# Kernel tuning notes

Measured on AMD Instinct MI355X. Metric: run time of the kernel, lower is better.

## Reference

```python
import jax, jax.numpy as jnp
import numpy as np

# hyper_params (mode='test')
PRE_NMS = 1000
POST_NMS = 300
IOU_TH = 0.7
VARIANCES = np.array([0.1, 0.1, 0.2, 0.2], dtype=np.float32)
FM = 64            # feature map height/width
ANCHOR_COUNT = 9   # 3 scales x 3 ratios


def _make_anchors():
    """Normalized [y1,x1,y2,x2] anchors on a FM x FM grid, 9 per cell."""
    scales = np.array([0.1, 0.2, 0.4], np.float32)
    ratios = np.array([0.5, 1.0, 2.0], np.float32)
    ws = (scales[:, None] * np.sqrt(ratios)[None, :]).reshape(-1)  # (9,)
    hs = (scales[:, None] / np.sqrt(ratios)[None, :]).reshape(-1)  # (9,)
    ctr = (np.arange(FM, dtype=np.float32) + 0.5) / FM
    cy, cx = np.meshgrid(ctr, ctr, indexing='ij')                  # (FM,FM)
    cy = cy[..., None]; cx = cx[..., None]                         # (FM,FM,1)
    anchors = np.stack([cy - 0.5 * hs, cx - 0.5 * ws,
                        cy + 0.5 * hs, cx + 0.5 * ws], axis=-1)    # (FM,FM,9,4)
    return jnp.asarray(anchors.reshape(-1, 4))                     # (36864,4)


def setup_inputs() -> dict:
    key = jax.random.key(0)
    k1, k2 = jax.random.split(key)
    B = 16
    rpn_bbox_deltas = jax.random.normal(k1, (B, FM, FM, ANCHOR_COUNT * 4), dtype=jnp.float32)
    rpn_labels = jax.random.uniform(k2, (B, FM, FM, ANCHOR_COUNT), dtype=jnp.float32)
    return {"rpn_bbox_deltas": rpn_bbox_deltas,
            "rpn_labels": rpn_labels,
            "anchors": _make_anchors()}


def _nms_single(boxes):
    """Greedy NMS on score-sorted boxes (N,4) -> (POST_NMS,4), zero-padded."""
    N = boxes.shape[0]
    y1, x1, y2, x2 = boxes[:, 0], boxes[:, 1], boxes[:, 2], boxes[:, 3]
    area = (y2 - y1) * (x2 - x1)                                   # (N,)
    iy1 = jnp.maximum(y1[:, None], y1[None, :])
    ix1 = jnp.maximum(x1[:, None], x1[None, :])
    iy2 = jnp.minimum(y2[:, None], y2[None, :])
    ix2 = jnp.minimum(x2[:, None], x2[None, :])
    inter = jnp.maximum(iy2 - iy1, 0.0) * jnp.maximum(ix2 - ix1, 0.0)
    iou = inter / jnp.maximum(area[:, None] + area[None, :] - inter, 1e-9)  # (N,N)
    idx = jnp.arange(N)

    def body(i, keep):
        # if box i survives, suppress later boxes with high overlap
        suppress = keep[i] & (iou[i] > IOU_TH) & (idx > i)
        return keep & ~suppress

    keep = jax.lax.fori_loop(0, N, body, jnp.ones((N,), dtype=bool))
    # stable sort: kept boxes first, original (score-descending) order preserved
    order = jnp.argsort(jnp.where(keep, 0, 1))[:POST_NMS]
    sel = boxes[order]
    valid = keep[order]
    # combined_non_max_suppression clips output boxes to [0,1] and zero-pads
    return jnp.where(valid[:, None], jnp.clip(sel, 0.0, 1.0), 0.0)


def reference(rpn_bbox_deltas, rpn_labels, anchors):
    B = rpn_bbox_deltas.shape[0]
    N = anchors.shape[0]
    deltas = rpn_bbox_deltas.reshape(B, N, 4) * jnp.asarray(VARIANCES)
    labels = rpn_labels.reshape(B, N)

    # decode deltas against anchors
    anc_h = anchors[:, 2] - anchors[:, 0]
    anc_w = anchors[:, 3] - anchors[:, 1]
    anc_cy = anchors[:, 0] + 0.5 * anc_h
    anc_cx = anchors[:, 1] + 0.5 * anc_w
    h = jnp.exp(deltas[..., 2]) * anc_h
    w = jnp.exp(deltas[..., 3]) * anc_w
    cy = deltas[..., 0] * anc_h + anc_cy
    cx = deltas[..., 1] * anc_w + anc_cx
    boxes = jnp.stack([cy - 0.5 * h, cx - 0.5 * w,
                       cy + 0.5 * h, cx + 0.5 * w], axis=-1)       # (B,N,4)

    # top-k by objectness score (descending, so NMS input is pre-sorted)
    _, pre_idx = jax.lax.top_k(labels, PRE_NMS)                    # (B,PRE_NMS)
    pre_boxes = jnp.take_along_axis(boxes, pre_idx[..., None], axis=1)  # (B,PRE_NMS,4)

    roi_bboxes = jax.vmap(_nms_single)(pre_boxes)                  # (B,POST_NMS,4)
    return jax.lax.stop_gradient(roi_bboxes)
```

## Files before the change

### kernel.cpp

```cpp
#include <hip/hip_runtime.h>
#include <stdint.h>

#pragma clang fp contract(off)

#define FM 64
#define AC 9
#define N_ANCH (FM * FM * AC)
#define PRE_NMS 1000
#define POST_NMS 300
#define SEL_CAP 1024
#define NWAVE 16

#define SLICES 16
#define K1_NT 256
#define SLICE_KEYS (N_ANCH / SLICES)
#define KEYS_PT (SLICE_KEYS / K1_NT)
#define SLICE_TOP 128
#define COMPACT_CAP 192
#define MERGE_CAP (SLICES * SLICE_TOP)

#define NCOPY 8
#define HSTR 257

#define M_WSTRIDE 1024
#define M_WORDS_PER_B (16 * M_WSTRIDE)
#define WS_BOX_FLOATS_PER_B (5 * SEL_CAP)

__device__ __forceinline__ uint32_t mono_key(float v) {
    uint32_t u = __float_as_uint(v);
    return (u & 0x80000000u) ? ~u : (u | 0x80000000u);
}

__device__ __forceinline__ float clip01(float x) {
    return fminf(fmaxf(x, 0.0f), 1.0f);
}

__device__ __forceinline__ uint64_t bcast64(uint64_t v, int srclane) {
    uint32_t lo = (uint32_t)v, hi = (uint32_t)(v >> 32);
    lo = __builtin_amdgcn_readlane(lo, srclane);
    hi = __builtin_amdgcn_readlane(hi, srclane);
    return ((uint64_t)hi << 32) | (uint64_t)lo;
}

__device__ __forceinline__ void scan256(const uint32_t* __restrict__ h, uint32_t K,
                                        uint32_t* shm, uint32_t& outBin, uint32_t& outKrem) {
    const int t    = threadIdx.x;
    const int lane = t & 63;
    const int wv   = t >> 6;
    const uint32_t q = h[t];
    uint32_t sfx = q, o;
    o = __shfl_down(sfx, 1);  if (lane < 63) sfx += o;
    o = __shfl_down(sfx, 2);  if (lane < 62) sfx += o;
    o = __shfl_down(sfx, 4);  if (lane < 60) sfx += o;
    o = __shfl_down(sfx, 8);  if (lane < 56) sfx += o;
    o = __shfl_down(sfx, 16); if (lane < 48) sfx += o;
    o = __shfl_down(sfx, 32); if (lane < 32) sfx += o;
    if (lane == 0) shm[wv] = sfx;
    __syncthreads();
    uint32_t wAbove = 0;
    for (int w2 = wv + 1; w2 < 4; ++w2) wAbove += shm[w2];
    const uint32_t above = wAbove + (sfx - q);
    if ((above < K) && (above + q >= K)) { shm[4] = (uint32_t)t; shm[5] = K - above; }
    __syncthreads();
    outBin  = shm[4];
    outKrem = shm[5];
}

__global__ __launch_bounds__(K1_NT) void k1s_slice_top(
    const float* __restrict__ labels,
    uint64_t* __restrict__ wsCand)
{
    const int s = blockIdx.x;
    const int b = blockIdx.y;
    const int t = threadIdx.x;
    const int lane = t & 63;

    __shared__ uint32_t hc[NCOPY * HSTR];
    __shared__ uint32_t red[256];
    __shared__ uint32_t shm[8];
    __shared__ uint64_t cand[COMPACT_CAP];
    __shared__ uint32_t scnt;

    const float* lab = labels + (size_t)b * N_ANCH + (size_t)s * SLICE_KEYS;
    uint32_t key[KEYS_PT];
#pragma unroll
    for (int r = 0; r < KEYS_PT; ++r)
        key[r] = mono_key(lab[r * K1_NT + t]);

    for (int i = t; i < NCOPY * HSTR; i += K1_NT) hc[i] = 0u;
    if (t == 0) scnt = 0u;
    __syncthreads();

    const int cbase = (lane & 7) * HSTR;
#pragma unroll
    for (int r = 0; r < KEYS_PT; ++r)
        atomicAdd(&hc[cbase + (key[r] >> 24)], 1u);
    __syncthreads();
    uint32_t sum = 0;
#pragma unroll
    for (int c = 0; c < NCOPY; ++c) sum += hc[c * HSTR + t];
    red[t] = sum;
    __syncthreads();
    uint32_t b0, krem;
    scan256(red, SLICE_TOP, shm, b0, krem);
    __syncthreads();

    red[t] = 0u;
    __syncthreads();
#pragma unroll
    for (int r = 0; r < KEYS_PT; ++r)
        if ((key[r] >> 24) == b0) atomicAdd(&red[(key[r] >> 16) & 0xFFu], 1u);
    __syncthreads();
    uint32_t b1, krem2;
    scan256(red, krem, shm, b1, krem2);
    const uint32_t thresh16 = (b0 << 8) | b1;

#pragma unroll
    for (int r = 0; r < KEYS_PT; ++r) {
        const uint32_t u = key[r];
        if ((u >> 16) >= thresh16) {
            const uint32_t gi = (uint32_t)(s * SLICE_KEYS + r * K1_NT + t);
            uint32_t pos = atomicAdd(&scnt, 1u);
            if (pos < COMPACT_CAP)
                cand[pos] = ((uint64_t)u << 32) | (uint64_t)(0xFFFFFFFFu - gi);
        }
    }
    __syncthreads();
    uint32_t c = scnt; if (c > COMPACT_CAP) c = COMPACT_CAP;
    if (t >= (int)c && t < COMPACT_CAP) cand[t] = 0ull;
    __syncthreads();

    if (t < COMPACT_CAP) {
        const uint64_t mine = cand[t];
        uint32_t rank = 0;
        for (int i = 0; i < COMPACT_CAP; i += 4) {
            rank += (cand[i]     > mine) + (cand[i + 1] > mine)
                  + (cand[i + 2] > mine) + (cand[i + 3] > mine);
        }
        if (t < (int)c && rank < SLICE_TOP)
            wsCand[((size_t)b * SLICES + s) * SLICE_TOP + rank] = mine;
    }
}

__global__ __launch_bounds__(K1_NT) void k1m_merge_decode(
    const float* __restrict__ deltas,
    const float* __restrict__ anchors,
    const uint64_t* __restrict__ wsCand,
    float* __restrict__ wsBox)
{
    const int chunk = blockIdx.x;
    const int b     = blockIdx.y;
    const int t     = threadIdx.x;

    __shared__ uint64_t keyA[MERGE_CAP];
    const uint64_t* c2 = wsCand + (size_t)b * MERGE_CAP;
    for (int i = t; i < MERGE_CAP; i += K1_NT) keyA[i] = c2[i];
    __syncthreads();

    if (t < SLICE_TOP) {
        const uint64_t mine = keyA[chunk * SLICE_TOP + t];
        uint32_t rank = 0;
#pragma unroll
        for (int r = 0; r < SLICES; ++r) {
            const uint64_t* a = &keyA[r * SLICE_TOP];
            uint32_t lo = 0;
#pragma unroll
            for (uint32_t s2 = 128; s2 > 0; s2 >>= 1)
                if (lo + s2 <= 128u && a[lo + s2 - 1] > mine) lo += s2;
            rank += lo;
        }
        if (rank < PRE_NMS) {
            uint32_t idx = 0xFFFFFFFFu - (uint32_t)(mine & 0xFFFFFFFFull);
            float4 d4 = *(const float4*)(deltas + ((size_t)b * N_ANCH + idx) * 4);
            float4 a4 = *(const float4*)(anchors + (size_t)idx * 4);
            float anc_h  = a4.z - a4.x;
            float anc_w  = a4.w - a4.y;
            float anc_cy = a4.x + 0.5f * anc_h;
            float anc_cx = a4.y + 0.5f * anc_w;
            float dy = d4.x * 0.1f, dx = d4.y * 0.1f;
            float dh = d4.z * 0.2f, dw = d4.w * 0.2f;
            float h  = expf(dh) * anc_h;
            float w  = expf(dw) * anc_w;
            float cy = dy * anc_h + anc_cy;
            float cx = dx * anc_w + anc_cx;
            float y1 = cy - 0.5f * h, x1 = cx - 0.5f * w;
            float y2 = cy + 0.5f * h, x2 = cx + 0.5f * w;
            float* wb = wsBox + (size_t)b * WS_BOX_FLOATS_PER_B;
            wb[rank]              = y1;
            wb[SEL_CAP + rank]    = x1;
            wb[2*SEL_CAP + rank]  = y2;
            wb[3*SEL_CAP + rank]  = x2;
            wb[4*SEL_CAP + rank]  = (y2 - y1) * (x2 - x1);
        }
    }
}

__global__ __launch_bounds__(1024) void k2_iou_matrix(
    const float* __restrict__ wsBox,
    uint64_t* __restrict__ wsM)
{
    const int gx   = blockIdx.x;
    const int b    = blockIdx.y;
    const int t    = threadIdx.x;
    const int lane = t & 63;
    const int wave = t >> 6;

    int cb, r0, r1;
    if (gx < 16) { cb = gx;     r0 = 0;   r1 = 64 * (cb + 1); if (r1 > 512) r1 = 512; }
    else         { cb = gx - 8; r0 = 512; r1 = 64 * (cb + 1); }
    if (r1 > PRE_NMS) r1 = PRE_NMS;

    __shared__ float s[5 * SEL_CAP];
    const float4* b4 = (const float4*)(wsBox + (size_t)b * WS_BOX_FLOATS_PER_B);
    float4* s4 = (float4*)s;
    for (int i = t; i < (5 * SEL_CAP) / 4; i += 1024) s4[i] = b4[i];
    __syncthreads();

    float* ly1 = s;
    float* lx1 = s + SEL_CAP;
    float* ly2 = s + 2 * SEL_CAP;
    float* lx2 = s + 3 * SEL_CAP;
    float* lar = s + 4 * SEL_CAP;

    const int j = cb * 64 + lane;
    const float y1j = ly1[j], x1j = lx1[j], y2j = ly2[j], x2j = lx2[j], aj = lar[j];

    uint64_t* Mb = wsM + (size_t)b * M_WORDS_PER_B + (size_t)cb * M_WSTRIDE;
    for (int i = r0 + wave; i < r1; i += NWAVE) {
        float iy1 = fmaxf(ly1[i], y1j);
        float ix1 = fmaxf(lx1[i], x1j);
        float iy2 = fminf(ly2[i], y2j);
        float ix2 = fminf(lx2[i], x2j);
        float ih = iy2 - iy1; if (ih < 0.f) ih = 0.f;
        float iw = ix2 - ix1; if (iw < 0.f) iw = 0.f;
        float inter = ih * iw;
        float denom = lar[i] + aj - inter;
        if (denom < 1e-9f) denom = 1e-9f;
        float iou = inter / denom;
        bool sup = (j > i) && (iou > 0.7f);
        uint64_t mask = __ballot(sup ? 1 : 0);
        if (lane == 0) Mb[i] = mask;
    }
}

__global__ __launch_bounds__(1024) void k3_reduce_out(
    const float* __restrict__ wsBox,
    const uint64_t* __restrict__ wsM,
    float* __restrict__ out)
{
    const int b    = blockIdx.x;
    const int t    = threadIdx.x;
    const int lane = t & 63;
    const int wave = t >> 6;

    __shared__ uint64_t remv[16];
    __shared__ uint64_t keepW[16];
    __shared__ uint32_t wordPref[16];

    const uint64_t* Mg = wsM + (size_t)b * M_WORDS_PER_B;

    if (t < 16) remv[t] = 0ull;
    __syncthreads();

    for (int w = 0; w < 16; ++w) {
        if (wave == 0) {
            const uint64_t m = Mg[(size_t)w * M_WSTRIDE + 64 * w + lane];
            uint64_t cur = remv[w];
            if (w < 15) {
#pragma unroll
                for (int bp = 0; bp < 64; ++bp) {
                    const uint64_t mb = bcast64(m, bp);
                    cur |= ((cur >> bp) & 1ull) ? 0ull : mb;
                }
            } else {
#pragma unroll
                for (int bp = 0; bp < 40; ++bp) {
                    const uint64_t mb = bcast64(m, bp);
                    cur |= ((cur >> bp) & 1ull) ? 0ull : mb;
                }
            }
            const uint64_t valid = (w == 15) ? ((1ull << 40) - 1ull) : ~0ull;
            if (lane == 0) keepW[w] = (~cur) & valid;
        }
        __syncthreads();
        if (wave > w) {
            const uint64_t km = keepW[w];
            uint64_t v = Mg[(size_t)wave * M_WSTRIDE + 64 * w + lane];
            v = ((km >> lane) & 1ull) ? v : 0ull;
            v |= __shfl_xor(v, 32);
            v |= __shfl_xor(v, 16);
            v |= __shfl_xor(v, 8);
            v |= __shfl_xor(v, 4);
            v |= __shfl_xor(v, 2);
            v |= __shfl_xor(v, 1);
            if (lane == 0) remv[wave] |= v;
        }
        __syncthreads();
    }

    if (t == 0) {
        uint32_t acc = 0u;
        for (int w = 0; w < 16; ++w) {
            wordPref[w] = acc;
            acc += (uint32_t)__popcll(keepW[w]);
        }
    }
    float* ob = out + (size_t)b * (POST_NMS * 4);
    for (int i = t; i < POST_NMS * 4; i += 1024) ob[i] = 0.0f;
    __syncthreads();

    if (t < PRE_NMS) {
        const int w = t >> 6, bpos = t & 63;
        uint64_t kw = keepW[w];
        if ((kw >> bpos) & 1ull) {
            uint32_t rank = wordPref[w] +
                            (uint32_t)__popcll(kw & ((1ull << bpos) - 1ull));
            if (rank < POST_NMS) {
                const float* wb = wsBox + (size_t)b * WS_BOX_FLOATS_PER_B;
                float* o = ob + (size_t)rank * 4;
                o[0] = clip01(wb[t]);
                o[1] = clip01(wb[SEL_CAP + t]);
                o[2] = clip01(wb[2*SEL_CAP + t]);
                o[3] = clip01(wb[3*SEL_CAP + t]);
            }
        }
    }
}

extern "C" void kernel_launch(void* const* d_in, const int* in_sizes, int n_in,
                              void* d_out, int out_size, void* d_ws, size_t ws_size,
                              hipStream_t stream) {
    const float* deltas  = (const float*)d_in[0];
    const float* labels  = (const float*)d_in[1];
    const float* anchors = (const float*)d_in[2];
    float* out = (float*)d_out;
    const int B = in_sizes[1] / N_ANCH;

    char* p = (char*)d_ws;
    uint64_t* wsCand = (uint64_t*)p;
    float*    wsBox  = (float*)(p + (size_t)B * MERGE_CAP * 8);
    uint64_t* wsM    = (uint64_t*)(p + (size_t)B * MERGE_CAP * 8
                                     + (size_t)B * WS_BOX_FLOATS_PER_B * 4);

    k1s_slice_top<<<dim3(SLICES, B), K1_NT, 0, stream>>>(labels, wsCand);
    k1m_merge_decode<<<dim3(SLICES, B), K1_NT, 0, stream>>>(deltas, anchors, wsCand, wsBox);
    k2_iou_matrix<<<dim3(24, B), 1024, 0, stream>>>(wsBox, wsM);
    k3_reduce_out<<<B, 1024, 0, stream>>>(wsBox, wsM, out);
}
```

Baseline: 131.0 us.

## Fuse top-k, decode, IoU and NMS reduce into one flag-synchronised kernel

Merges the four separate launches into one kernel with 16 blocks per image. The stages are ordered by per-image global flags that each block writes with release stores and polls with acquire loads. The aim is to remove launch gaps and let different images progress independently. The IoU stage also shrinks from 1024-thread blocks to 256-thread blocks, which lowers per-image parallelism. The flags are set to a magic value and never cleared, so repeated calls on the same workspace could pass the waits early unless the workspace is zeroed between calls.

```diff
diff --git a/kernel.cpp b/kernel.cpp
--- a/kernel.cpp
+++ b/kernel.cpp
@@ -3,28 +3,28 @@
 
 #pragma clang fp contract(off)
 
-#define FM 64
-#define AC 9
-#define N_ANCH (FM * FM * AC)
+#define N_ANCH 36864
 #define PRE_NMS 1000
 #define POST_NMS 300
 #define SEL_CAP 1024
-#define NWAVE 16
+#define NT 256
 
 #define SLICES 16
-#define K1_NT 256
-#define SLICE_KEYS (N_ANCH / SLICES)
-#define KEYS_PT (SLICE_KEYS / K1_NT)
+#define SLICE_KEYS 2304
+#define KEYS_PT 9
 #define SLICE_TOP 128
 #define COMPACT_CAP 192
-#define MERGE_CAP (SLICES * SLICE_TOP)
+#define MERGE_CAP 2048
 
 #define NCOPY 8
 #define HSTR 257
 
 #define M_WSTRIDE 1024
-#define M_WORDS_PER_B (16 * M_WSTRIDE)
-#define WS_BOX_FLOATS_PER_B (5 * SEL_CAP)
+#define M_WORDS_PER_B 16384
+#define WS_BOX_FLOATS_PER_B 5120
+
+#define MAGIC 0x5CA1AB1Eu
+#define SMEM_BYTES 20992
 
 __device__ __forceinline__ uint32_t mono_key(float v) {
     uint32_t u = __float_as_uint(v);
@@ -40,6 +40,27 @@
     lo = __builtin_amdgcn_readlane(lo, srclane);
     hi = __builtin_amdgcn_readlane(hi, srclane);
     return ((uint64_t)hi << 32) | (uint64_t)lo;
+}
+
+__device__ __forceinline__ void signal(uint32_t* f) {
+    __syncthreads();
+    if (threadIdx.x == 0) {
+        __threadfence();
+        __hip_atomic_store(f, MAGIC, __ATOMIC_RELEASE, __HIP_MEMORY_SCOPE_AGENT);
+    }
+}
+
+__device__ __forceinline__ void wait16(const uint32_t* fbase) {
+    const int t = threadIdx.x;
+    int ok;
+    do {
+        ok = 1;
+        if (t < 16)
+            ok = (__hip_atomic_load(&fbase[t], __ATOMIC_ACQUIRE,
+                                    __HIP_MEMORY_SCOPE_AGENT) == MAGIC);
+        else
+            __builtin_amdgcn_s_sleep(2);
+    } while (!__syncthreads_and(ok));
 }
 
 __device__ __forceinline__ void scan256(const uint32_t* __restrict__ h, uint32_t K,
@@ -66,262 +87,256 @@
     outKrem = shm[5];
 }
 
-__global__ __launch_bounds__(K1_NT) void k1s_slice_top(
+__global__ __launch_bounds__(NT) void fused_roibbox(
+    const float* __restrict__ deltas,
     const float* __restrict__ labels,
-    uint64_t* __restrict__ wsCand)
+    const float* __restrict__ anchors,
+    float* __restrict__ out,
+    uint64_t* __restrict__ wsCand,
+    float* __restrict__ wsBox,
+    uint64_t* __restrict__ wsM,
+    uint32_t* __restrict__ wsFlag,
+    int nB)
 {
-    const int s = blockIdx.x;
-    const int b = blockIdx.y;
-    const int t = threadIdx.x;
-    const int lane = t & 63;
-
-    __shared__ uint32_t hc[NCOPY * HSTR];
-    __shared__ uint32_t red[256];
-    __shared__ uint32_t shm[8];
-    __shared__ uint64_t cand[COMPACT_CAP];
-    __shared__ uint32_t scnt;
-
-    const float* lab = labels + (size_t)b * N_ANCH + (size_t)s * SLICE_KEYS;
-    uint32_t key[KEYS_PT];
-#pragma unroll
-    for (int r = 0; r < KEYS_PT; ++r)
-        key[r] = mono_key(lab[r * K1_NT + t]);
-
-    for (int i = t; i < NCOPY * HSTR; i += K1_NT) hc[i] = 0u;
-    if (t == 0) scnt = 0u;
-    __syncthreads();
-
-    const int cbase = (lane & 7) * HSTR;
-#pragma unroll
-    for (int r = 0; r < KEYS_PT; ++r)
-        atomicAdd(&hc[cbase + (key[r] >> 24)], 1u);
-    __syncthreads();
-    uint32_t sum = 0;
-#pragma unroll
-    for (int c = 0; c < NCOPY; ++c) sum += hc[c * HSTR + t];
-    red[t] = sum;
-    __syncthreads();
-    uint32_t b0, krem;
-    scan256(red, SLICE_TOP, shm, b0, krem);
-    __syncthreads();
-
-    red[t] = 0u;
-    __syncthreads();
-#pragma unroll
-    for (int r = 0; r < KEYS_PT; ++r)
-        if ((key[r] >> 24) == b0) atomicAdd(&red[(key[r] >> 16) & 0xFFu], 1u);
-    __syncthreads();
-    uint32_t b1, krem2;
-    scan256(red, krem, shm, b1, krem2);
-    const uint32_t thresh16 = (b0 << 8) | b1;
-
-#pragma unroll
-    for (int r = 0; r < KEYS_PT; ++r) {
-        const uint32_t u = key[r];
-        if ((u >> 16) >= thresh16) {
-            const uint32_t gi = (uint32_t)(s * SLICE_KEYS + r * K1_NT + t);
-            uint32_t pos = atomicAdd(&scnt, 1u);
-            if (pos < COMPACT_CAP)
-                cand[pos] = ((uint64_t)u << 32) | (uint64_t)(0xFFFFFFFFu - gi);
-        }
-    }
-    __syncthreads();
-    uint32_t c = scnt; if (c > COMPACT_CAP) c = COMPACT_CAP;
-    if (t >= (int)c && t < COMPACT_CAP) cand[t] = 0ull;
-    __syncthreads();
-
-    if (t < COMPACT_CAP) {
-        const uint64_t mine = cand[t];
-        uint32_t rank = 0;
-        for (int i = 0; i < COMPACT_CAP; i += 4) {
-            rank += (cand[i]     > mine) + (cand[i + 1] > mine)
-                  + (cand[i + 2] > mine) + (cand[i + 3] > mine);
-        }
-        if (t < (int)c && rank < SLICE_TOP)
-            wsCand[((size_t)b * SLICES + s) * SLICE_TOP + rank] = mine;
-    }
-}
-
-__global__ __launch_bounds__(K1_NT) void k1m_merge_decode(
-    const float* __restrict__ deltas,
-    const float* __restrict__ anchors,
-    const uint64_t* __restrict__ wsCand,
-    float* __restrict__ wsBox)
-{
-    const int chunk = blockIdx.x;
-    const int b     = blockIdx.y;
+    extern __shared__ char sm[];
+    const int bid   = blockIdx.x;
+    const int chunk = bid & 15;
+    const int b     = bid >> 4;
     const int t     = threadIdx.x;
-
-    __shared__ uint64_t keyA[MERGE_CAP];
-    const uint64_t* c2 = wsCand + (size_t)b * MERGE_CAP;
-    for (int i = t; i < MERGE_CAP; i += K1_NT) keyA[i] = c2[i];
-    __syncthreads();
-
-    if (t < SLICE_TOP) {
-        const uint64_t mine = keyA[chunk * SLICE_TOP + t];
-        uint32_t rank = 0;
-#pragma unroll
-        for (int r = 0; r < SLICES; ++r) {
-            const uint64_t* a = &keyA[r * SLICE_TOP];
-            uint32_t lo = 0;
-#pragma unroll
-            for (uint32_t s2 = 128; s2 > 0; s2 >>= 1)
-                if (lo + s2 <= 128u && a[lo + s2 - 1] > mine) lo += s2;
-            rank += lo;
-        }
-        if (rank < PRE_NMS) {
-            uint32_t idx = 0xFFFFFFFFu - (uint32_t)(mine & 0xFFFFFFFFull);
-            float4 d4 = *(const float4*)(deltas + ((size_t)b * N_ANCH + idx) * 4);
-            float4 a4 = *(const float4*)(anchors + (size_t)idx * 4);
-            float anc_h  = a4.z - a4.x;
-            float anc_w  = a4.w - a4.y;
-            float anc_cy = a4.x + 0.5f * anc_h;
-            float anc_cx = a4.y + 0.5f * anc_w;
-            float dy = d4.x * 0.1f, dx = d4.y * 0.1f;
-            float dh = d4.z * 0.2f, dw = d4.w * 0.2f;
-            float h  = expf(dh) * anc_h;
-            float w  = expf(dw) * anc_w;
-            float cy = dy * anc_h + anc_cy;
-            float cx = dx * anc_w + anc_cx;
-            float y1 = cy - 0.5f * h, x1 = cx - 0.5f * w;
-            float y2 = cy + 0.5f * h, x2 = cx + 0.5f * w;
-            float* wb = wsBox + (size_t)b * WS_BOX_FLOATS_PER_B;
-            wb[rank]              = y1;
-            wb[SEL_CAP + rank]    = x1;
-            wb[2*SEL_CAP + rank]  = y2;
-            wb[3*SEL_CAP + rank]  = x2;
-            wb[4*SEL_CAP + rank]  = (y2 - y1) * (x2 - x1);
-        }
-    }
-}
-
-__global__ __launch_bounds__(1024) void k2_iou_matrix(
-    const float* __restrict__ wsBox,
-    uint64_t* __restrict__ wsM)
-{
-    const int gx   = blockIdx.x;
-    const int b    = blockIdx.y;
-    const int t    = threadIdx.x;
-    const int lane = t & 63;
-    const int wave = t >> 6;
-
-    int cb, r0, r1;
-    if (gx < 16) { cb = gx;     r0 = 0;   r1 = 64 * (cb + 1); if (r1 > 512) r1 = 512; }
-    else         { cb = gx - 8; r0 = 512; r1 = 64 * (cb + 1); }
-    if (r1 > PRE_NMS) r1 = PRE_NMS;
-
-    __shared__ float s[5 * SEL_CAP];
-    const float4* b4 = (const float4*)(wsBox + (size_t)b * WS_BOX_FLOATS_PER_B);
-    float4* s4 = (float4*)s;
-    for (int i = t; i < (5 * SEL_CAP) / 4; i += 1024) s4[i] = b4[i];
-    __syncthreads();
-
-    float* ly1 = s;
-    float* lx1 = s + SEL_CAP;
-    float* ly2 = s + 2 * SEL_CAP;
-    float* lx2 = s + 3 * SEL_CAP;
-    float* lar = s + 4 * SEL_CAP;
-
-    const int j = cb * 64 + lane;
-    const float y1j = ly1[j], x1j = lx1[j], y2j = ly2[j], x2j = lx2[j], aj = lar[j];
-
-    uint64_t* Mb = wsM + (size_t)b * M_WORDS_PER_B + (size_t)cb * M_WSTRIDE;
-    for (int i = r0 + wave; i < r1; i += NWAVE) {
-        float iy1 = fmaxf(ly1[i], y1j);
-        float ix1 = fmaxf(lx1[i], x1j);
-        float iy2 = fminf(ly2[i], y2j);
-        float ix2 = fminf(lx2[i], x2j);
-        float ih = iy2 - iy1; if (ih < 0.f) ih = 0.f;
-        float iw = ix2 - ix1; if (iw < 0.f) iw = 0.f;
-        float inter = ih * iw;
-        float denom = lar[i] + aj - inter;
-        if (denom < 1e-9f) denom = 1e-9f;
-        float iou = inter / denom;
-        bool sup = (j > i) && (iou > 0.7f);
-        uint64_t mask = __ballot(sup ? 1 : 0);
-        if (lane == 0) Mb[i] = mask;
-    }
-}
-
-__global__ __launch_bounds__(1024) void k3_reduce_out(
-    const float* __restrict__ wsBox,
-    const uint64_t* __restrict__ wsM,
-    float* __restrict__ out)
-{
-    const int b    = blockIdx.x;
-    const int t    = threadIdx.x;
-    const int lane = t & 63;
-    const int wave = t >> 6;
-
-    __shared__ uint64_t remv[16];
-    __shared__ uint64_t keepW[16];
-    __shared__ uint32_t wordPref[16];
-
-    const uint64_t* Mg = wsM + (size_t)b * M_WORDS_PER_B;
-
-    if (t < 16) remv[t] = 0ull;
-    __syncthreads();
-
-    for (int w = 0; w < 16; ++w) {
-        if (wave == 0) {
-            const uint64_t m = Mg[(size_t)w * M_WSTRIDE + 64 * w + lane];
-            uint64_t cur = remv[w];
-            if (w < 15) {
-#pragma unroll
-                for (int bp = 0; bp < 64; ++bp) {
-                    const uint64_t mb = bcast64(m, bp);
-                    cur |= ((cur >> bp) & 1ull) ? 0ull : mb;
+    const int lane  = t & 63;
+    const int wave  = t >> 6;
+
+    uint32_t* flagA = wsFlag + b * 16;
+    uint32_t* flagB = wsFlag + (nB + b) * 16;
+    uint32_t* flagC = wsFlag + (2 * nB + b) * 16;
+
+    {
+        uint32_t* hc   = (uint32_t*)sm;
+        uint32_t* red  = (uint32_t*)(sm + 8224);
+        uint32_t* shm  = (uint32_t*)(sm + 9248);
+        uint64_t* cand = (uint64_t*)(sm + 9280);
+        uint32_t* scnt = (uint32_t*)(sm + 10816);
+
+        const float* lab = labels + (size_t)b * N_ANCH + (size_t)chunk * SLICE_KEYS;
+        uint32_t key[KEYS_PT];
+#pragma unroll
+        for (int r = 0; r < KEYS_PT; ++r)
+            key[r] = mono_key(lab[r * NT + t]);
+
+        for (int i = t; i < NCOPY * HSTR; i += NT) hc[i] = 0u;
+        if (t == 0) *scnt = 0u;
+        __syncthreads();
+
+        const int cbase = (lane & 7) * HSTR;
+#pragma unroll
+        for (int r = 0; r < KEYS_PT; ++r)
+            atomicAdd(&hc[cbase + (key[r] >> 24)], 1u);
+        __syncthreads();
+        uint32_t sum = 0;
+#pragma unroll
+        for (int c = 0; c < NCOPY; ++c) sum += hc[c * HSTR + t];
+        red[t] = sum;
+        __syncthreads();
+        uint32_t b0, krem;
+        scan256(red, SLICE_TOP, shm, b0, krem);
+        __syncthreads();
+
+        red[t] = 0u;
+        __syncthreads();
+#pragma unroll
+        for (int r = 0; r < KEYS_PT; ++r)
+            if ((key[r] >> 24) == b0) atomicAdd(&red[(key[r] >> 16) & 0xFFu], 1u);
+        __syncthreads();
+        uint32_t b1, krem2;
+        scan256(red, krem, shm, b1, krem2);
+        const uint32_t thresh16 = (b0 << 8) | b1;
+
+#pragma unroll
+        for (int r = 0; r < KEYS_PT; ++r) {
+            const uint32_t u = key[r];
+            if ((u >> 16) >= thresh16) {
+                const uint32_t gi = (uint32_t)(chunk * SLICE_KEYS + r * NT + t);
+                uint32_t pos = atomicAdd(scnt, 1u);
+                if (pos < COMPACT_CAP)
+                    cand[pos] = ((uint64_t)u << 32) | (uint64_t)(0xFFFFFFFFu - gi);
+            }
+        }
+        __syncthreads();
+        uint32_t c = *scnt; if (c > COMPACT_CAP) c = COMPACT_CAP;
+        if (t >= (int)c && t < COMPACT_CAP) cand[t] = 0ull;
+        __syncthreads();
+
+        if (t < COMPACT_CAP) {
+            const uint64_t mine = cand[t];
+            uint32_t rank = 0;
+            for (int i = 0; i < COMPACT_CAP; i += 4)
+                rank += (cand[i]     > mine) + (cand[i + 1] > mine)
+                      + (cand[i + 2] > mine) + (cand[i + 3] > mine);
+            if (t < (int)c && rank < SLICE_TOP)
+                wsCand[((size_t)b * SLICES + chunk) * SLICE_TOP + rank] = mine;
+        }
+    }
+    signal(&flagA[chunk]);
+
+    wait16(flagA);
+    {
+        uint64_t* keyA = (uint64_t*)sm;
+        const uint64_t* c2 = wsCand + (size_t)b * MERGE_CAP;
+        for (int i = t; i < MERGE_CAP; i += NT) keyA[i] = c2[i];
+        __syncthreads();
+
+        if (t < SLICE_TOP) {
+            const uint64_t mine = keyA[chunk * SLICE_TOP + t];
+            uint32_t rank = 0;
+#pragma unroll
+            for (int r = 0; r < SLICES; ++r) {
+                const uint64_t* a = &keyA[r * SLICE_TOP];
+                uint32_t lo = 0;
+#pragma unroll
+                for (uint32_t s2 = 128; s2 > 0; s2 >>= 1)
+                    if (lo + s2 <= 128u && a[lo + s2 - 1] > mine) lo += s2;
+                rank += lo;
+            }
+            if (rank < PRE_NMS) {
+                uint32_t idx = 0xFFFFFFFFu - (uint32_t)(mine & 0xFFFFFFFFull);
+                float4 d4 = *(const float4*)(deltas + ((size_t)b * N_ANCH + idx) * 4);
+                float4 a4 = *(const float4*)(anchors + (size_t)idx * 4);
+                float anc_h  = a4.z - a4.x;
+                float anc_w  = a4.w - a4.y;
+                float anc_cy = a4.x + 0.5f * anc_h;
+                float anc_cx = a4.y + 0.5f * anc_w;
+                float dy = d4.x * 0.1f, dx = d4.y * 0.1f;
+                float dh = d4.z * 0.2f, dw = d4.w * 0.2f;
+                float h  = expf(dh) * anc_h;
+                float w  = expf(dw) * anc_w;
+                float cy = dy * anc_h + anc_cy;
+                float cx = dx * anc_w + anc_cx;
+                float y1 = cy - 0.5f * h, x1 = cx - 0.5f * w;
+                float y2 = cy + 0.5f * h, x2 = cx + 0.5f * w;
+                float* wb = wsBox + (size_t)b * WS_BOX_FLOATS_PER_B;
+                wb[rank]              = y1;
+                wb[SEL_CAP + rank]    = x1;
+                wb[2*SEL_CAP + rank]  = y2;
+                wb[3*SEL_CAP + rank]  = x2;
+                wb[4*SEL_CAP + rank]  = (y2 - y1) * (x2 - x1);
+            }
+        }
+    }
+    signal(&flagB[chunk]);
+
+    wait16(flagB);
+    {
+        float* sbox = (float*)sm;
+        const float4* b4 = (const float4*)(wsBox + (size_t)b * WS_BOX_FLOATS_PER_B);
+        float4* s4 = (float4*)sbox;
+        for (int i = t; i < WS_BOX_FLOATS_PER_B / 4; i += NT) s4[i] = b4[i];
+        __syncthreads();
+
+        float* ly1 = sbox;
+        float* lx1 = sbox + SEL_CAP;
+        float* ly2 = sbox + 2 * SEL_CAP;
+        float* lx2 = sbox + 3 * SEL_CAP;
+        float* lar = sbox + 4 * SEL_CAP;
+
+        const int j = chunk * 64 + lane;
+        const float y1j = ly1[j], x1j = lx1[j], y2j = ly2[j], x2j = lx2[j], aj = lar[j];
+
+        int r1 = 64 * (chunk + 1);
+        if (r1 > PRE_NMS) r1 = PRE_NMS;
+        uint64_t* Mb = wsM + (size_t)b * M_WORDS_PER_B + (size_t)chunk * M_WSTRIDE;
+
+        for (int i = wave; i < r1; i += 4) {
+            float iy1 = fmaxf(ly1[i], y1j);
+            float ix1 = fmaxf(lx1[i], x1j);
+            float iy2 = fminf(ly2[i], y2j);
+            float ix2 = fminf(lx2[i], x2j);
+            float ih = iy2 - iy1; if (ih < 0.f) ih = 0.f;
+            float iw = ix2 - ix1; if (iw < 0.f) iw = 0.f;
+            float inter = ih * iw;
+            float denom = lar[i] + aj - inter;
+            if (denom < 1e-9f) denom = 1e-9f;
+            float iou = inter / denom;
+            bool sup = (j > i) && (iou > 0.7f);
+            uint64_t mask = __ballot(sup ? 1 : 0);
+            if (lane == 0) Mb[i] = mask;
+        }
+    }
+    signal(&flagC[chunk]);
+
+    if (chunk != 0) return;
+    wait16(flagC);
+    {
+        uint64_t* remv     = (uint64_t*)sm;
+        uint64_t* keepW    = remv + 16;
+        uint32_t* wordPref = (uint32_t*)(keepW + 16);
+
+        const uint64_t* Mg = wsM + (size_t)b * M_WORDS_PER_B;
+        if (t < 16) remv[t] = 0ull;
+        __syncthreads();
+
+        for (int w = 0; w < 16; ++w) {
+            if (wave == 0) {
+                const uint64_t m = Mg[(size_t)w * M_WSTRIDE + 64 * w + lane];
+                uint64_t cur = remv[w];
+                if (w < 15) {
+#pragma unroll
+                    for (int bp = 0; bp < 64; ++bp) {
+                        const uint64_t mb = bcast64(m, bp);
+                        cur |= ((cur >> bp) & 1ull) ? 0ull : mb;
+                    }
+                } else {
+#pragma unroll
+                    for (int bp = 0; bp < 40; ++bp) {
+                        const uint64_t mb = bcast64(m, bp);
+                        cur |= ((cur >> bp) & 1ull) ? 0ull : mb;
+                    }
                 }
-            } else {
-#pragma unroll
-                for (int bp = 0; bp < 40; ++bp) {
-                    const uint64_t mb = bcast64(m, bp);
-                    cur |= ((cur >> bp) & 1ull) ? 0ull : mb;
+                const uint64_t valid = (w == 15) ? ((1ull << 40) - 1ull) : ~0ull;
+                if (lane == 0) keepW[w] = (~cur) & valid;
+            }
+            __syncthreads();
+            if (wave > 0) {
+                const uint64_t km = keepW[w];
+                for (int w2 = w + wave; w2 < 16; w2 += 3) {
+                    uint64_t v = Mg[(size_t)w2 * M_WSTRIDE + 64 * w + lane];
+                    v = ((km >> lane) & 1ull) ? v : 0ull;
+                    v |= __shfl_xor(v, 32);
+                    v |= __shfl_xor(v, 16);
+                    v |= __shfl_xor(v, 8);
+                    v |= __shfl_xor(v, 4);
+                    v |= __shfl_xor(v, 2);
+                    v |= __shfl_xor(v, 1);
+                    if (lane == 0) remv[w2] |= v;
                 }
             }
-            const uint64_t valid = (w == 15) ? ((1ull << 40) - 1ull) : ~0ull;
-            if (lane == 0) keepW[w] = (~cur) & valid;
-        }
-        __syncthreads();
-        if (wave > w) {
-            const uint64_t km = keepW[w];
-            uint64_t v = Mg[(size_t)wave * M_WSTRIDE + 64 * w + lane];
-            v = ((km >> lane) & 1ull) ? v : 0ull;
-            v |= __shfl_xor(v, 32);
-            v |= __shfl_xor(v, 16);
-            v |= __shfl_xor(v, 8);
-            v |= __shfl_xor(v, 4);
-            v |= __shfl_xor(v, 2);
-            v |= __shfl_xor(v, 1);
-            if (lane == 0) remv[wave] |= v;
-        }
-        __syncthreads();
-    }
-
-    if (t == 0) {
-        uint32_t acc = 0u;
-        for (int w = 0; w < 16; ++w) {
-            wordPref[w] = acc;
-            acc += (uint32_t)__popcll(keepW[w]);
-        }
-    }
-    float* ob = out + (size_t)b * (POST_NMS * 4);
-    for (int i = t; i < POST_NMS * 4; i += 1024) ob[i] = 0.0f;
-    __syncthreads();
-
-    if (t < PRE_NMS) {
-        const int w = t >> 6, bpos = t & 63;
-        uint64_t kw = keepW[w];
-        if ((kw >> bpos) & 1ull) {
-            uint32_t rank = wordPref[w] +
-                            (uint32_t)__popcll(kw & ((1ull << bpos) - 1ull));
-            if (rank < POST_NMS) {
-                const float* wb = wsBox + (size_t)b * WS_BOX_FLOATS_PER_B;
-                float* o = ob + (size_t)rank * 4;
-                o[0] = clip01(wb[t]);
-                o[1] = clip01(wb[SEL_CAP + t]);
-                o[2] = clip01(wb[2*SEL_CAP + t]);
-                o[3] = clip01(wb[3*SEL_CAP + t]);
+            __syncthreads();
+        }
+
+        if (t == 0) {
+            uint32_t acc = 0u;
+            for (int w = 0; w < 16; ++w) {
+                wordPref[w] = acc;
+                acc += (uint32_t)__popcll(keepW[w]);
+            }
+        }
+        float* ob = out + (size_t)b * (POST_NMS * 4);
+        for (int i = t; i < POST_NMS * 4; i += NT) ob[i] = 0.0f;
+        __syncthreads();
+
+        const float* wb = wsBox + (size_t)b * WS_BOX_FLOATS_PER_B;
+        for (int q = t; q < PRE_NMS; q += NT) {
+            const int w = q >> 6, bpos = q & 63;
+            uint64_t kw = keepW[w];
+            if ((kw >> bpos) & 1ull) {
+                uint32_t rank = wordPref[w] +
+                                (uint32_t)__popcll(kw & ((1ull << bpos) - 1ull));
+                if (rank < POST_NMS) {
+                    float* o = ob + (size_t)rank * 4;
+                    o[0] = clip01(wb[q]);
+                    o[1] = clip01(wb[SEL_CAP + q]);
+                    o[2] = clip01(wb[2*SEL_CAP + q]);
+                    o[3] = clip01(wb[3*SEL_CAP + q]);
+                }
             }
         }
     }
@@ -341,9 +356,10 @@
     float*    wsBox  = (float*)(p + (size_t)B * MERGE_CAP * 8);
     uint64_t* wsM    = (uint64_t*)(p + (size_t)B * MERGE_CAP * 8
                                      + (size_t)B * WS_BOX_FLOATS_PER_B * 4);
-
-    k1s_slice_top<<<dim3(SLICES, B), K1_NT, 0, stream>>>(labels, wsCand);
-    k1m_merge_decode<<<dim3(SLICES, B), K1_NT, 0, stream>>>(deltas, anchors, wsCand, wsBox);
-    k2_iou_matrix<<<dim3(24, B), 1024, 0, stream>>>(wsBox, wsM);
-    k3_reduce_out<<<B, 1024, 0, stream>>>(wsBox, wsM, out);
-}
+    uint32_t* wsFlag = (uint32_t*)(p + (size_t)B * MERGE_CAP * 8
+                                     + (size_t)B * WS_BOX_FLOATS_PER_B * 4
+                                     + (size_t)B * M_WORDS_PER_B * 8);
+
+    fused_roibbox<<<dim3(SLICES * B), dim3(NT), SMEM_BYTES, stream>>>(
+        deltas, labels, anchors, out, wsCand, wsBox, wsM, wsFlag, B);
+}
```

Result: slower. 205.5 us (+56.8%).

## Fuse merge-decode, IoU matrix and NMS reduction into one per-batch kernel

Applied to the files above, without the earlier changes.

Replaces three kernels (merge/decode, IoU bitmask, greedy reduce) with a single 1024-thread block per image that keeps candidate keys, decoded boxes and the full suppression bitmask in ~150KB of LDS. This removes two kernel launches and the global-memory round trips for boxes and the mask matrix. The cost is parallelism: only B=16 blocks run instead of 16×B and 24×B, so the IoU work is spread over far fewer CUs. It also adds a large LDS zero-fill.

```diff
diff --git a/kernel.cpp b/kernel.cpp
--- a/kernel.cpp
+++ b/kernel.cpp
@@ -3,9 +3,7 @@
 
 #pragma clang fp contract(off)
 
-#define FM 64
-#define AC 9
-#define N_ANCH (FM * FM * AC)
+#define N_ANCH 36864
 #define PRE_NMS 1000
 #define POST_NMS 300
 #define SEL_CAP 1024
@@ -13,18 +11,19 @@
 
 #define SLICES 16
 #define K1_NT 256
-#define SLICE_KEYS (N_ANCH / SLICES)
-#define KEYS_PT (SLICE_KEYS / K1_NT)
+#define SLICE_KEYS 2304
+#define KEYS_PT 9
 #define SLICE_TOP 128
 #define COMPACT_CAP 192
-#define MERGE_CAP (SLICES * SLICE_TOP)
+#define MERGE_CAP 2048
 
 #define NCOPY 8
 #define HSTR 257
 
-#define M_WSTRIDE 1024
-#define M_WORDS_PER_B (16 * M_WSTRIDE)
-#define WS_BOX_FLOATS_PER_B (5 * SEL_CAP)
+#define M_OFF   0
+#define BOX_OFF 131072
+#define SC_OFF  151552
+#define KBIG_SMEM 152064
 
 __device__ __forceinline__ uint32_t mono_key(float v) {
     uint32_t u = __float_as_uint(v);
@@ -133,32 +132,48 @@
     if (t < COMPACT_CAP) {
         const uint64_t mine = cand[t];
         uint32_t rank = 0;
-        for (int i = 0; i < COMPACT_CAP; i += 4) {
+        for (int i = 0; i < COMPACT_CAP; i += 4)
             rank += (cand[i]     > mine) + (cand[i + 1] > mine)
                   + (cand[i + 2] > mine) + (cand[i + 3] > mine);
-        }
         if (t < (int)c && rank < SLICE_TOP)
             wsCand[((size_t)b * SLICES + s) * SLICE_TOP + rank] = mine;
     }
 }
 
-__global__ __launch_bounds__(K1_NT) void k1m_merge_decode(
+__global__ __launch_bounds__(1024) void kbig(
     const float* __restrict__ deltas,
     const float* __restrict__ anchors,
     const uint64_t* __restrict__ wsCand,
-    float* __restrict__ wsBox)
+    float* __restrict__ out)
 {
-    const int chunk = blockIdx.x;
-    const int b     = blockIdx.y;
-    const int t     = threadIdx.x;
-
-    __shared__ uint64_t keyA[MERGE_CAP];
+    extern __shared__ char sm[];
+    uint64_t* Mlds  = (uint64_t*)sm;
+    float*    boxes = (float*)(sm + BOX_OFF);
+    uint64_t* remv  = (uint64_t*)(sm + SC_OFF);
+    uint64_t* keepW = remv + 16;
+    uint32_t* wordPref = (uint32_t*)(keepW + 16);
+    uint64_t* keyA  = Mlds;
+
+    const int b    = blockIdx.x;
+    const int t    = threadIdx.x;
+    const int lane = t & 63;
+    const int wave = t >> 6;
+
+    float* ly1 = boxes;
+    float* lx1 = boxes + SEL_CAP;
+    float* ly2 = boxes + 2 * SEL_CAP;
+    float* lx2 = boxes + 3 * SEL_CAP;
+    float* lar = boxes + 4 * SEL_CAP;
+
     const uint64_t* c2 = wsCand + (size_t)b * MERGE_CAP;
-    for (int i = t; i < MERGE_CAP; i += K1_NT) keyA[i] = c2[i];
-    __syncthreads();
-
-    if (t < SLICE_TOP) {
-        const uint64_t mine = keyA[chunk * SLICE_TOP + t];
+    keyA[t]        = c2[t];
+    keyA[t + 1024] = c2[t + 1024];
+    for (int i = t; i < 5 * SEL_CAP; i += 1024) boxes[i] = 0.f;
+    __syncthreads();
+
+#pragma unroll
+    for (int kk = 0; kk < 2; ++kk) {
+        const uint64_t mine = keyA[t + kk * 1024];
         uint32_t rank = 0;
 #pragma unroll
         for (int r = 0; r < SLICES; ++r) {
@@ -185,86 +200,50 @@
             float cx = dx * anc_w + anc_cx;
             float y1 = cy - 0.5f * h, x1 = cx - 0.5f * w;
             float y2 = cy + 0.5f * h, x2 = cx + 0.5f * w;
-            float* wb = wsBox + (size_t)b * WS_BOX_FLOATS_PER_B;
-            wb[rank]              = y1;
-            wb[SEL_CAP + rank]    = x1;
-            wb[2*SEL_CAP + rank]  = y2;
-            wb[3*SEL_CAP + rank]  = x2;
-            wb[4*SEL_CAP + rank]  = (y2 - y1) * (x2 - x1);
-        }
-    }
-}
-
-__global__ __launch_bounds__(1024) void k2_iou_matrix(
-    const float* __restrict__ wsBox,
-    uint64_t* __restrict__ wsM)
-{
-    const int gx   = blockIdx.x;
-    const int b    = blockIdx.y;
-    const int t    = threadIdx.x;
-    const int lane = t & 63;
-    const int wave = t >> 6;
-
-    int cb, r0, r1;
-    if (gx < 16) { cb = gx;     r0 = 0;   r1 = 64 * (cb + 1); if (r1 > 512) r1 = 512; }
-    else         { cb = gx - 8; r0 = 512; r1 = 64 * (cb + 1); }
-    if (r1 > PRE_NMS) r1 = PRE_NMS;
-
-    __shared__ float s[5 * SEL_CAP];
-    const float4* b4 = (const float4*)(wsBox + (size_t)b * WS_BOX_FLOATS_PER_B);
-    float4* s4 = (float4*)s;
-    for (int i = t; i < (5 * SEL_CAP) / 4; i += 1024) s4[i] = b4[i];
-    __syncthreads();
-
-    float* ly1 = s;
-    float* lx1 = s + SEL_CAP;
-    float* ly2 = s + 2 * SEL_CAP;
-    float* lx2 = s + 3 * SEL_CAP;
-    float* lar = s + 4 * SEL_CAP;
-
-    const int j = cb * 64 + lane;
-    const float y1j = ly1[j], x1j = lx1[j], y2j = ly2[j], x2j = lx2[j], aj = lar[j];
-
-    uint64_t* Mb = wsM + (size_t)b * M_WORDS_PER_B + (size_t)cb * M_WSTRIDE;
-    for (int i = r0 + wave; i < r1; i += NWAVE) {
-        float iy1 = fmaxf(ly1[i], y1j);
-        float ix1 = fmaxf(lx1[i], x1j);
-        float iy2 = fminf(ly2[i], y2j);
-        float ix2 = fminf(lx2[i], x2j);
-        float ih = iy2 - iy1; if (ih < 0.f) ih = 0.f;
-        float iw = ix2 - ix1; if (iw < 0.f) iw = 0.f;
-        float inter = ih * iw;
-        float denom = lar[i] + aj - inter;
-        if (denom < 1e-9f) denom = 1e-9f;
-        float iou = inter / denom;
-        bool sup = (j > i) && (iou > 0.7f);
-        uint64_t mask = __ballot(sup ? 1 : 0);
-        if (lane == 0) Mb[i] = mask;
-    }
-}
-
-__global__ __launch_bounds__(1024) void k3_reduce_out(
-    const float* __restrict__ wsBox,
-    const uint64_t* __restrict__ wsM,
-    float* __restrict__ out)
-{
-    const int b    = blockIdx.x;
-    const int t    = threadIdx.x;
-    const int lane = t & 63;
-    const int wave = t >> 6;
-
-    __shared__ uint64_t remv[16];
-    __shared__ uint64_t keepW[16];
-    __shared__ uint32_t wordPref[16];
-
-    const uint64_t* Mg = wsM + (size_t)b * M_WORDS_PER_B;
+            ly1[rank] = y1; lx1[rank] = x1; ly2[rank] = y2; lx2[rank] = x2;
+            lar[rank] = (y2 - y1) * (x2 - x1);
+        }
+    }
+    __syncthreads();
+
+    for (int i = t; i < 16 * 1024; i += 1024) Mlds[i] = 0ull;
+    __syncthreads();
+
+    {
+        const int p = wave >> 1, half = wave & 1;
+#pragma unroll
+        for (int sel = 0; sel < 2; ++sel) {
+            const int w = sel ? (15 - p) : p;
+            const int j = (w << 6) | lane;
+            const float y1j = ly1[j], x1j = lx1[j], y2j = ly2[j], x2j = lx2[j], aj = lar[j];
+            int rmax = (w + 1) << 6; if (rmax > PRE_NMS) rmax = PRE_NMS;
+            const int rbeg = half ? (rmax >> 1) : 0;
+            const int rend = half ? rmax : (rmax >> 1);
+            for (int i = rbeg; i < rend; ++i) {
+                float iy1 = fmaxf(ly1[i], y1j);
+                float ix1 = fmaxf(lx1[i], x1j);
+                float iy2 = fminf(ly2[i], y2j);
+                float ix2 = fminf(lx2[i], x2j);
+                float ih = iy2 - iy1; if (ih < 0.f) ih = 0.f;
+                float iw = ix2 - ix1; if (iw < 0.f) iw = 0.f;
+                float inter = ih * iw;
+                float denom = lar[i] + aj - inter;
+                if (denom < 1e-9f) denom = 1e-9f;
+                float iou = inter / denom;
+                bool sup = (j > i) && (iou > 0.7f);
+                uint64_t mask = __ballot(sup ? 1 : 0);
+                if (lane == 0) Mlds[(w << 10) + i] = mask;
+            }
+        }
+    }
+    __syncthreads();
 
     if (t < 16) remv[t] = 0ull;
     __syncthreads();
 
     for (int w = 0; w < 16; ++w) {
         if (wave == 0) {
-            const uint64_t m = Mg[(size_t)w * M_WSTRIDE + 64 * w + lane];
+            const uint64_t m = Mlds[(w << 10) + 64 * w + lane];
             uint64_t cur = remv[w];
             if (w < 15) {
 #pragma unroll
@@ -285,7 +264,7 @@
         __syncthreads();
         if (wave > w) {
             const uint64_t km = keepW[w];
-            uint64_t v = Mg[(size_t)wave * M_WSTRIDE + 64 * w + lane];
+            uint64_t v = Mlds[(wave << 10) + 64 * w + lane];
             v = ((km >> lane) & 1ull) ? v : 0ull;
             v |= __shfl_xor(v, 32);
             v |= __shfl_xor(v, 16);
@@ -316,12 +295,11 @@
             uint32_t rank = wordPref[w] +
                             (uint32_t)__popcll(kw & ((1ull << bpos) - 1ull));
             if (rank < POST_NMS) {
-                const float* wb = wsBox + (size_t)b * WS_BOX_FLOATS_PER_B;
                 float* o = ob + (size_t)rank * 4;
-                o[0] = clip01(wb[t]);
-                o[1] = clip01(wb[SEL_CAP + t]);
-                o[2] = clip01(wb[2*SEL_CAP + t]);
-                o[3] = clip01(wb[3*SEL_CAP + t]);
+                o[0] = clip01(ly1[t]);
+                o[1] = clip01(lx1[t]);
+                o[2] = clip01(ly2[t]);
+                o[3] = clip01(lx2[t]);
             }
         }
     }
@@ -336,14 +314,8 @@
     float* out = (float*)d_out;
     const int B = in_sizes[1] / N_ANCH;
 
-    char* p = (char*)d_ws;
-    uint64_t* wsCand = (uint64_t*)p;
-    float*    wsBox  = (float*)(p + (size_t)B * MERGE_CAP * 8);
-    uint64_t* wsM    = (uint64_t*)(p + (size_t)B * MERGE_CAP * 8
-                                     + (size_t)B * WS_BOX_FLOATS_PER_B * 4);
+    uint64_t* wsCand = (uint64_t*)d_ws;
 
     k1s_slice_top<<<dim3(SLICES, B), K1_NT, 0, stream>>>(labels, wsCand);
-    k1m_merge_decode<<<dim3(SLICES, B), K1_NT, 0, stream>>>(deltas, anchors, wsCand, wsBox);
-    k2_iou_matrix<<<dim3(24, B), 1024, 0, stream>>>(wsBox, wsM);
-    k3_reduce_out<<<B, 1024, 0, stream>>>(wsBox, wsM, out);
-}
+    kbig<<<B, 1024, KBIG_SMEM, stream>>>(deltas, anchors, wsCand, out);
+}
```

Result: slower. 273.9 us (+109.0%).

## Fuse merge-rank/decode into IOU matrix kernel, decoding boxes into shared memory

Applied to the files above, without the earlier changes.

Removes the separate merge/decode kernel. Each of the 24 IOU-matrix blocks per batch now recomputes the global rank of all 2048 candidates and decodes the top-1000 boxes straight into shared memory. Block 0 writes the box coordinates to the workspace for the final kernel. This drops one kernel launch and a global round trip of the box data, at the cost of redundant rank and decode work in every block. The area array is no longer written to the workspace, so k3 must not depend on it.

```diff
diff --git a/kernel.cpp b/kernel.cpp
--- a/kernel.cpp
+++ b/kernel.cpp
@@ -3,9 +3,7 @@
 
 #pragma clang fp contract(off)
 
-#define FM 64
-#define AC 9
-#define N_ANCH (FM * FM * AC)
+#define N_ANCH 36864
 #define PRE_NMS 1000
 #define POST_NMS 300
 #define SEL_CAP 1024
@@ -13,18 +11,18 @@
 
 #define SLICES 16
 #define K1_NT 256
-#define SLICE_KEYS (N_ANCH / SLICES)
-#define KEYS_PT (SLICE_KEYS / K1_NT)
+#define SLICE_KEYS 2304
+#define KEYS_PT 9
 #define SLICE_TOP 128
 #define COMPACT_CAP 192
-#define MERGE_CAP (SLICES * SLICE_TOP)
+#define MERGE_CAP 2048
 
 #define NCOPY 8
 #define HSTR 257
 
 #define M_WSTRIDE 1024
-#define M_WORDS_PER_B (16 * M_WSTRIDE)
-#define WS_BOX_FLOATS_PER_B (5 * SEL_CAP)
+#define M_WORDS_PER_B 16384
+#define WS_BOX_FLOATS_PER_B 5120
 
 __device__ __forceinline__ uint32_t mono_key(float v) {
     uint32_t u = __float_as_uint(v);
@@ -133,32 +131,49 @@
     if (t < COMPACT_CAP) {
         const uint64_t mine = cand[t];
         uint32_t rank = 0;
-        for (int i = 0; i < COMPACT_CAP; i += 4) {
+        for (int i = 0; i < COMPACT_CAP; i += 4)
             rank += (cand[i]     > mine) + (cand[i + 1] > mine)
                   + (cand[i + 2] > mine) + (cand[i + 3] > mine);
-        }
         if (t < (int)c && rank < SLICE_TOP)
             wsCand[((size_t)b * SLICES + s) * SLICE_TOP + rank] = mine;
     }
 }
 
-__global__ __launch_bounds__(K1_NT) void k1m_merge_decode(
+__global__ __launch_bounds__(1024) void k2_rank_matrix(
     const float* __restrict__ deltas,
     const float* __restrict__ anchors,
     const uint64_t* __restrict__ wsCand,
-    float* __restrict__ wsBox)
+    float* __restrict__ wsBox,
+    uint64_t* __restrict__ wsM)
 {
-    const int chunk = blockIdx.x;
-    const int b     = blockIdx.y;
-    const int t     = threadIdx.x;
-
     __shared__ uint64_t keyA[MERGE_CAP];
+    __shared__ float    boxes[5 * SEL_CAP];
+
+    const int gx   = blockIdx.x;
+    const int b    = blockIdx.y;
+    const int t    = threadIdx.x;
+    const int lane = t & 63;
+    const int wave = t >> 6;
+
+    int cb, r0, r1;
+    if (gx < 16) { cb = gx;     r0 = 0;   r1 = 64 * (cb + 1); if (r1 > 512) r1 = 512; }
+    else         { cb = gx - 8; r0 = 512; r1 = 64 * (cb + 1); }
+    if (r1 > PRE_NMS) r1 = PRE_NMS;
+
+    float* ly1 = boxes;
+    float* lx1 = boxes + SEL_CAP;
+    float* ly2 = boxes + 2 * SEL_CAP;
+    float* lx2 = boxes + 3 * SEL_CAP;
+    float* lar = boxes + 4 * SEL_CAP;
+
     const uint64_t* c2 = wsCand + (size_t)b * MERGE_CAP;
-    for (int i = t; i < MERGE_CAP; i += K1_NT) keyA[i] = c2[i];
-    __syncthreads();
-
-    if (t < SLICE_TOP) {
-        const uint64_t mine = keyA[chunk * SLICE_TOP + t];
+    keyA[t]        = c2[t];
+    keyA[t + 1024] = c2[t + 1024];
+    __syncthreads();
+
+#pragma unroll
+    for (int kk = 0; kk < 2; ++kk) {
+        const uint64_t mine = keyA[t + kk * 1024];
         uint32_t rank = 0;
 #pragma unroll
         for (int r = 0; r < SLICES; ++r) {
@@ -185,42 +200,21 @@
             float cx = dx * anc_w + anc_cx;
             float y1 = cy - 0.5f * h, x1 = cx - 0.5f * w;
             float y2 = cy + 0.5f * h, x2 = cx + 0.5f * w;
-            float* wb = wsBox + (size_t)b * WS_BOX_FLOATS_PER_B;
-            wb[rank]              = y1;
-            wb[SEL_CAP + rank]    = x1;
-            wb[2*SEL_CAP + rank]  = y2;
-            wb[3*SEL_CAP + rank]  = x2;
-            wb[4*SEL_CAP + rank]  = (y2 - y1) * (x2 - x1);
-        }
-    }
-}
-
-__global__ __launch_bounds__(1024) void k2_iou_matrix(
-    const float* __restrict__ wsBox,
-    uint64_t* __restrict__ wsM)
-{
-    const int gx   = blockIdx.x;
-    const int b    = blockIdx.y;
-    const int t    = threadIdx.x;
-    const int lane = t & 63;
-    const int wave = t >> 6;
-
-    int cb, r0, r1;
-    if (gx < 16) { cb = gx;     r0 = 0;   r1 = 64 * (cb + 1); if (r1 > 512) r1 = 512; }
-    else         { cb = gx - 8; r0 = 512; r1 = 64 * (cb + 1); }
-    if (r1 > PRE_NMS) r1 = PRE_NMS;
-
-    __shared__ float s[5 * SEL_CAP];
-    const float4* b4 = (const float4*)(wsBox + (size_t)b * WS_BOX_FLOATS_PER_B);
-    float4* s4 = (float4*)s;
-    for (int i = t; i < (5 * SEL_CAP) / 4; i += 1024) s4[i] = b4[i];
-    __syncthreads();
-
-    float* ly1 = s;
-    float* lx1 = s + SEL_CAP;
-    float* ly2 = s + 2 * SEL_CAP;
-    float* lx2 = s + 3 * SEL_CAP;
-    float* lar = s + 4 * SEL_CAP;
+            ly1[rank] = y1; lx1[rank] = x1; ly2[rank] = y2; lx2[rank] = x2;
+            lar[rank] = (y2 - y1) * (x2 - x1);
+        }
+    }
+    __syncthreads();
+
+    if (gx == 0) {
+        float* wb = wsBox + (size_t)b * WS_BOX_FLOATS_PER_B;
+        for (int i = t; i < PRE_NMS; i += 1024) {
+            wb[i]               = ly1[i];
+            wb[SEL_CAP + i]     = lx1[i];
+            wb[2 * SEL_CAP + i] = ly2[i];
+            wb[3 * SEL_CAP + i] = lx2[i];
+        }
+    }
 
     const int j = cb * 64 + lane;
     const float y1j = ly1[j], x1j = lx1[j], y2j = ly2[j], x2j = lx2[j], aj = lar[j];
@@ -343,7 +337,6 @@
                                      + (size_t)B * WS_BOX_FLOATS_PER_B * 4);
 
     k1s_slice_top<<<dim3(SLICES, B), K1_NT, 0, stream>>>(labels, wsCand);
-    k1m_merge_decode<<<dim3(SLICES, B), K1_NT, 0, stream>>>(deltas, anchors, wsCand, wsBox);
-    k2_iou_matrix<<<dim3(24, B), 1024, 0, stream>>>(wsBox, wsM);
+    k2_rank_matrix<<<dim3(24, B), 1024, 0, stream>>>(deltas, anchors, wsCand, wsBox, wsM);
     k3_reduce_out<<<B, 1024, 0, stream>>>(wsBox, wsM, out);
 }
```

New measurement: 139.9 us. 6.8% more time.
